# Optimization experiments

Measured on AMD Instinct MI355X. Metric: run time of the kernel, lower is better.

Reference implementation:

```python
import jax, jax.numpy as jnp
from jax import lax
import numpy as np

B, C_IN, C_OUT, H, MODES, L = 16, 128, 128, 8, 256, 16384
HEAD_IN, HEAD_OUT = C_IN // H, C_OUT // H


def setup_inputs() -> dict:
    key = jax.random.key(0)
    ks = jax.random.split(key, 6)
    init_std = (2.0 / (C_IN + C_OUT)) ** 0.5
    return {
        "x": jax.random.normal(ks[0], (B, C_IN, L), dtype=jnp.float32),
        "weight_re": init_std * jax.random.normal(ks[1], (H, HEAD_IN, HEAD_OUT, MODES), dtype=jnp.float32),
        "weight_im": init_std * jax.random.normal(ks[2], (H, HEAD_IN, HEAD_OUT, MODES), dtype=jnp.float32),
        "bias": init_std * jax.random.normal(ks[3], (C_OUT, 1), dtype=jnp.float32),
        "conv_w": (1.0 / np.sqrt(C_IN * 3)) * jax.random.normal(ks[4], (C_OUT, C_IN, 3), dtype=jnp.float32),
        "conv_b": (1.0 / np.sqrt(C_IN * 3)) * jax.random.normal(ks[5], (C_OUT,), dtype=jnp.float32),
        "gate": jnp.array(0.0, dtype=jnp.float32),
    }


def reference(x, weight_re, weight_im, bias, conv_w, conv_b, gate):
    b, _, n = x.shape
    # rfft with norm='forward' (forward transform scaled by 1/n)
    x_freq = jnp.fft.rfft(x, axis=-1, norm="forward")            # (b, C_IN, n//2+1) complex
    x_freq = x_freq.reshape(b, H, HEAD_IN, -1)                    # (b, h, i, f)
    w = weight_re + 1j * weight_im                                # (h, i, o, MODES)
    # truncated low-frequency complex mixing per head
    out_freq = jnp.einsum("bhif,hiof->bhof", x_freq[..., :MODES], w)
    out_freq = out_freq.reshape(b, C_OUT, MODES)
    # irfft zero-pads the truncated spectrum back to n//2+1 modes
    x_out = jnp.fft.irfft(out_freq, n=n, axis=-1, norm="forward")  # (b, C_OUT, n) real
    x_out = x_out + bias                                           # bias: (C_OUT, 1)
    # local conv branch: Conv1d(kernel=3, padding=1) == SAME
    local = lax.conv_general_dilated(
        x, conv_w, window_strides=(1,), padding="SAME",
        dimension_numbers=("NCH", "OIH", "NCH"),
    ) + conv_b[None, :, None]
    g = jax.nn.sigmoid(gate)
    return g * x_out + (1.0 - g) * local
```

## Files before the change

kernel.cpp:

```cpp
#include <hip/hip_runtime.h>


typedef __bf16 bf16x8 __attribute__((ext_vector_type(8)));
typedef __bf16 bf16x4 __attribute__((ext_vector_type(4)));
typedef float f32x4 __attribute__((ext_vector_type(4)));
typedef unsigned short ushort8v __attribute__((ext_vector_type(8)));

#define PI2_OVER_L 3.8349519697141029073e-4f

__global__ void genF_kern(__bf16* __restrict__ Fjt) {
    unsigned idx = blockIdx.x * 256u + threadIdx.x;
    unsigned k = idx >> 14, t = idx & 16383u;
    unsigned m = (k * t) & 16383u;
    float th = (float)m * PI2_OVER_L;
    float s, c;
    __sincosf(th, &s, &c);
    const float inv = 1.0f / 16384.0f;
    Fjt[((size_t)(2u * k) << 14) + t]      = (__bf16)(c * inv);
    Fjt[((size_t)(2u * k + 1u) << 14) + t] = (__bf16)(-s * inv);
}

__global__ void genG_kern(__bf16* __restrict__ Gtj, const float* __restrict__ gate, int fold) {
    unsigned idx = blockIdx.x * 256u + threadIdx.x;
    unsigned t = idx >> 8, k = idx & 255u;
    unsigned m = (k * t) & 16383u;
    float th = (float)m * PI2_OVER_L;
    float s, c;
    __sincosf(th, &s, &c);
    float a = (k == 0u) ? 1.0f : 2.0f;
    if (fold) a *= 1.0f / (1.0f + __expf(-gate[0]));
    size_t base = ((size_t)t << 9) + 2u * k;
    Gtj[base]     = (__bf16)(a * c);
    Gtj[base + 1] = (__bf16)(-a * s);
}

__global__ void wcvt_kern(const float* __restrict__ cw, __bf16* __restrict__ wbf,
                          const float* __restrict__ gate, int fold) {
    int idx = blockIdx.x * 256 + threadIdx.x;
    float sc = 1.0f;
    if (fold) sc = 1.0f - 1.0f / (1.0f + __expf(-gate[0]));
    int co = idx / 384, r = idx - co * 384, ci = r / 3, d = r - ci * 3;
    wbf[d * 16384 + co * 128 + ci] = (__bf16)(cw[idx] * sc);
}

__global__ __launch_bounds__(256) void xpose_kern(const float* __restrict__ x,
        __bf16* __restrict__ xb, __bf16* __restrict__ xTb, int write_xb) {
    __shared__ __bf16 tile[128 * 68];
    int bid = blockIdx.x;
    int b = bid >> 8, tB = bid & 255, t0 = tB << 6;
    int tid = threadIdx.x;
    for (int idx = tid; idx < 2048; idx += 256) {
        int ci = idx >> 4, ch = idx & 15;
        size_t gp = ((size_t)((b << 7) + ci) << 14) + t0 + (ch << 2);
        float4 v = *(const float4*)(x + gp);
        bf16x4 p;
        p[0] = (__bf16)v.x; p[1] = (__bf16)v.y; p[2] = (__bf16)v.z; p[3] = (__bf16)v.w;
        *(bf16x4*)&tile[ci * 68 + (ch << 2)] = p;
        if (write_xb) *(bf16x4*)(xb + gp) = p;
    }
    __syncthreads();
    for (int idx = tid; idx < 1024; idx += 256) {
        int t = idx >> 4, ch = idx & 15;
        bf16x8 v;
#pragma unroll
        for (int j = 0; j < 8; j++) v[j] = tile[(ch * 8 + j) * 68 + t];
        *(bf16x8*)(xTb + (((size_t)(b << 14)) + t0 + t) * 128 + ch * 8) = v;
    }
}

#define SA 72
template<int ABF>
__global__ __launch_bounds__(256) void fwd_kern(const float* __restrict__ xf,
        const __bf16* __restrict__ xbv, const __bf16* __restrict__ Fjt,
        float* __restrict__ Cp, int kchunk) {
    __shared__ __align__(16) __bf16 As[128 * SA];
    __shared__ __align__(16) __bf16 Bs[128 * SA];
    int bid = blockIdx.x;
    int mt = bid & 15, nt = (bid >> 4) & 3, ks = bid >> 6;
    int tid = threadIdx.x, lane = tid & 63, wv = tid >> 6;
    int wm = (wv >> 1) << 6, wn = (wv & 1) << 6;
    f32x4 acc[4][4] = {};
    int arow = tid >> 1, ahalf = (tid & 1) << 5;
    const float*  agf = xf  + ((size_t)(mt * 128 + arow) << 14) + ahalf;
    const __bf16* agb = xbv + ((size_t)(mt * 128 + arow) << 14) + ahalf;
    const __bf16* bg  = Fjt + ((size_t)(nt * 128 + arow) << 14) + ahalf;
    __bf16* ad = &As[arow * SA + ahalf];
    __bf16* bd = &Bs[arow * SA + ahalf];
    int k0 = ks * kchunk;
    for (int kk = 0; kk < kchunk; kk += 64) {
        if (ABF) {
            const ushort8v* ap = (const ushort8v*)(agb + k0 + kk);
#pragma unroll
            for (int q = 0; q < 4; q++) ((ushort8v*)ad)[q] = ap[q];
        } else {
            const float4* ap = (const float4*)(agf + k0 + kk);
#pragma unroll
            for (int q = 0; q < 8; q++) {
                float4 v = ap[q];
                ad[q * 4 + 0] = (__bf16)v.x; ad[q * 4 + 1] = (__bf16)v.y;
                ad[q * 4 + 2] = (__bf16)v.z; ad[q * 4 + 3] = (__bf16)v.w;
            }
        }
        const ushort8v* bp = (const ushort8v*)(bg + k0 + kk);
#pragma unroll
        for (int q = 0; q < 4; q++) ((ushort8v*)bd)[q] = bp[q];
        __syncthreads();
#pragma unroll
        for (int ks2 = 0; ks2 < 64; ks2 += 32) {
            int kf = ks2 + ((lane >> 4) << 3);
            bf16x8 af[4], bfv[4];
#pragma unroll
            for (int i = 0; i < 4; i++)
                af[i] = *(const bf16x8*)&As[(wm + i * 16 + (lane & 15)) * SA + kf];
#pragma unroll
            for (int j = 0; j < 4; j++)
                bfv[j] = *(const bf16x8*)&Bs[(wn + j * 16 + (lane & 15)) * SA + kf];
#pragma unroll
            for (int i = 0; i < 4; i++)
#pragma unroll
                for (int j = 0; j < 4; j++)
                    acc[i][j] = __builtin_amdgcn_mfma_f32_16x16x32_bf16(af[i], bfv[j], acc[i][j], 0, 0, 0);
        }
        __syncthreads();
    }
    float* outp = Cp + (size_t)ks * (2048 * 512);
    int q = lane >> 4, cl = lane & 15;
#pragma unroll
    for (int i = 0; i < 4; i++)
#pragma unroll
        for (int j = 0; j < 4; j++) {
            int col = nt * 128 + wn + j * 16 + cl;
#pragma unroll
            for (int r = 0; r < 4; r++) {
                int row = mt * 128 + wm + i * 16 + q * 4 + r;
                outp[(size_t)row * 512 + col] = acc[i][j][r];
            }
        }
}

__global__ __launch_bounds__(256) void mix_kern(const float* __restrict__ Cp,
        const float* __restrict__ wre, const float* __restrict__ wim,
        __bf16* __restrict__ Ob, int ns) {
    __shared__ float Fs[16 * 256];
    int bid = blockIdx.x, bh = bid >> 1, kh = bid & 1;
    int b = bh >> 3, h = bh & 7;
    int tid = threadIdx.x;
    size_t base = (size_t)(b * 128 + h * 16) * 512 + kh * 256;
    for (int idx = tid; idx < 4096; idx += 256) {
        int i = idx >> 8, jj = idx & 255;
        float v = 0.f;
        for (int s = 0; s < ns; s++) v += Cp[(size_t)s * 1048576 + base + (size_t)i * 512 + jj];
        Fs[i * 256 + jj] = v;
    }
    __syncthreads();
    for (int idx = tid; idx < 2048; idx += 256) {
        int o = idx >> 7, kl = idx & 127;
        int k = kh * 128 + kl;
        float ar = 0.f, ai = 0.f;
        const float* wr0 = wre + ((size_t)(h * 256 + o) << 8) + k;
        const float* wi0 = wim + ((size_t)(h * 256 + o) << 8) + k;
#pragma unroll 4
        for (int i = 0; i < 16; i++) {
            float fr = Fs[i * 256 + 2 * kl], fi = Fs[i * 256 + 2 * kl + 1];
            float wr = wr0[(size_t)i * 4096], wi = wi0[(size_t)i * 4096];
            ar += fr * wr - fi * wi;
            ai += fr * wi + fi * wr;
        }
        size_t ro = (size_t)(b * 128 + h * 16 + o) * 512;
        Ob[ro + 2 * k]     = (__bf16)ar;
        Ob[ro + 2 * k + 1] = (__bf16)ai;
    }
}

#define SC 72
__global__ __launch_bounds__(256) void fused_kern(const __bf16* __restrict__ Ob,
        const __bf16* __restrict__ Gtj, const __bf16* __restrict__ wbf,
        const __bf16* __restrict__ xTb, const float* __restrict__ bias,
        const float* __restrict__ cb, const float* __restrict__ gate,
        float* __restrict__ out) {
    __shared__ __align__(16) char smem[37152];
    int bid = blockIdx.x, b = bid & 15, tt = bid >> 4;
    int t0 = tt << 7;
    int tid = threadIdx.x, lane = tid & 63, wv = tid >> 6;
    int wm = (wv >> 1) << 6, wn = (wv & 1) << 6, lm = lane & 15;
    f32x4 acc[4][4] = {};

    {
        __bf16* As = (__bf16*)smem;
        __bf16* Bs = (__bf16*)(smem + 128 * SA * 2);
        int arow = tid >> 1, ahalf = (tid & 1) << 5;
        const __bf16* ag = Ob  + (size_t)(b * 128 + arow) * 512 + ahalf;
        const __bf16* bg = Gtj + (size_t)(tt * 128 + arow) * 512 + ahalf;
        __bf16* ad = &As[arow * SA + ahalf];
        __bf16* bd = &Bs[arow * SA + ahalf];
        for (int k0 = 0; k0 < 512; k0 += 64) {
#pragma unroll
            for (int q = 0; q < 4; q++) {
                ((ushort8v*)ad)[q] = ((const ushort8v*)(ag + k0))[q];
                ((ushort8v*)bd)[q] = ((const ushort8v*)(bg + k0))[q];
            }
            __syncthreads();
#pragma unroll
            for (int ks2 = 0; ks2 < 64; ks2 += 32) {
                int kf = ks2 + ((lane >> 4) << 3);
                bf16x8 af[4], bfv[4];
#pragma unroll
                for (int i = 0; i < 4; i++)
                    af[i] = *(const bf16x8*)&As[(wm + i * 16 + lm) * SA + kf];
#pragma unroll
                for (int j = 0; j < 4; j++)
                    bfv[j] = *(const bf16x8*)&Bs[(wn + j * 16 + lm) * SA + kf];
#pragma unroll
                for (int i = 0; i < 4; i++)
#pragma unroll
                    for (int j = 0; j < 4; j++)
                        acc[i][j] = __builtin_amdgcn_mfma_f32_16x16x32_bf16(af[i], bfv[j], acc[i][j], 0, 0, 0);
            }
            __syncthreads();
        }
    }

    {
        __bf16* xT = (__bf16*)smem;
        __bf16* Ws = (__bf16*)(smem + 130 * SC * 2);
        for (int c0p = 0; c0p < 2; c0p++) {
            int c0 = c0p << 6;
            if (c0p) __syncthreads();
            for (int idx = tid; idx < 1040; idx += 256) {
                int row = idx >> 3, ch = idx & 7;
                int tg = t0 - 1 + row;
                ushort8v v = {};
                if (tg >= 0 && tg < 16384)
                    v = *(const ushort8v*)(xTb + (((size_t)(b << 14)) + tg) * 128 + c0 + ch * 8);
                *(ushort8v*)&xT[row * SC + ch * 8] = v;
            }
            for (int d = 0; d < 3; d++) {
                if (d) __syncthreads();
                for (int idx = tid; idx < 1024; idx += 256) {
                    int co = idx >> 3, ch = idx & 7;
                    *(ushort8v*)&Ws[co * SC + ch * 8] =
                        *(const ushort8v*)(wbf + d * 16384 + co * 128 + c0 + ch * 8);
                }
                __syncthreads();
#pragma unroll
                for (int ks2 = 0; ks2 < 64; ks2 += 32) {
                    int kf = ks2 + ((lane >> 4) << 3);
                    bf16x8 af[4], bfv[4];
#pragma unroll
                    for (int i = 0; i < 4; i++)
                        af[i] = *(const bf16x8*)&Ws[(wm + i * 16 + lm) * SC + kf];
#pragma unroll
                    for (int j = 0; j < 4; j++)
                        bfv[j] = *(const bf16x8*)&xT[(wn + j * 16 + lm + d) * SC + kf];
#pragma unroll
                    for (int i = 0; i < 4; i++)
#pragma unroll
                        for (int j = 0; j < 4; j++)
                            acc[i][j] = __builtin_amdgcn_mfma_f32_16x16x32_bf16(af[i], bfv[j], acc[i][j], 0, 0, 0);
                }
            }
        }
    }

    float g = 1.0f / (1.0f + __expf(-gate[0]));
    int q = lane >> 4, cl = lane & 15;
#pragma unroll
    for (int i = 0; i < 4; i++)
#pragma unroll
        for (int j = 0; j < 4; j++) {
            int t = t0 + wn + j * 16 + cl;
#pragma unroll
            for (int r = 0; r < 4; r++) {
                int co = wm + i * 16 + q * 4 + r;
                float gb = g * bias[co] + (1.0f - g) * cb[co];
                out[((size_t)(b * 128 + co) << 14) + t] = acc[i][j][r] + gb;
            }
        }
}

#define SXC 40
__global__ __launch_bounds__(256) void conv_kern(const float* __restrict__ x,
        const __bf16* __restrict__ wbf, const float* __restrict__ cb,
        float* __restrict__ out) {
    __shared__ __align__(16) __bf16 xT[130 * SXC];
    __shared__ __align__(16) __bf16 wS[3 * 128 * SXC];
    int bid = blockIdx.x, b = bid >> 7, t0 = (bid & 127) << 7;
    int tid = threadIdx.x, lane = tid & 63, wv = tid >> 6;
    int wm = (wv >> 1) << 6, wn = (wv & 1) << 6;
    f32x4 acc[4][4] = {};
    for (int c0 = 0; c0 < 128; c0 += 32) {
        for (int idx = tid; idx < 1536; idx += 256) {
            int d = idx / 512, rem = idx - d * 512, co = rem >> 2, g = rem & 3;
            ushort8v v = *(const ushort8v*)(wbf + d * 16384 + co * 128 + c0 + g * 8);
            *(ushort8v*)&wS[d * (128 * SXC) + co * SXC + g * 8] = v;
        }
        for (int idx = tid; idx < 4160; idx += 256) {
            int cc = idx / 130, tl = idx - cc * 130;
            int tg = t0 + tl - 1;
            float v = 0.f;
            if (tg >= 0 && tg < 16384)
                v = x[((size_t)(b * 128 + c0 + cc) << 14) + tg];
            xT[tl * SXC + cc] = (__bf16)v;
        }
        __syncthreads();
        int kf = (lane >> 4) << 3;
#pragma unroll
        for (int d = 0; d < 3; d++) {
            bf16x8 af[4], bfv[4];
#pragma unroll
            for (int i = 0; i < 4; i++)
                af[i] = *(const bf16x8*)&wS[d * (128 * SXC) + (wm + i * 16 + (lane & 15)) * SXC + kf];
#pragma unroll
            for (int j = 0; j < 4; j++)
                bfv[j] = *(const bf16x8*)&xT[(wn + j * 16 + (lane & 15) + d) * SXC + kf];
#pragma unroll
            for (int i = 0; i < 4; i++)
#pragma unroll
                for (int j = 0; j < 4; j++)
                    acc[i][j] = __builtin_amdgcn_mfma_f32_16x16x32_bf16(af[i], bfv[j], acc[i][j], 0, 0, 0);
        }
        __syncthreads();
    }
    int q = lane >> 4, cl = lane & 15;
#pragma unroll
    for (int i = 0; i < 4; i++)
#pragma unroll
        for (int j = 0; j < 4; j++) {
            int t = t0 + wn + j * 16 + cl;
#pragma unroll
            for (int r = 0; r < 4; r++) {
                int co = wm + i * 16 + q * 4 + r;
                out[((size_t)(b * 128 + co) << 14) + t] = acc[i][j][r] + cb[co];
            }
        }
}

__global__ __launch_bounds__(256) void inv_kern(const __bf16* __restrict__ Ob,
        const __bf16* __restrict__ Gtj, const float* __restrict__ bias,
        const float* __restrict__ gate, float* __restrict__ out) {
    __shared__ __align__(16) __bf16 As[128 * SA];
    __shared__ __align__(16) __bf16 Bs[128 * SA];
    int bid = blockIdx.x, mt = bid & 15, tt = bid >> 4;
    int tid = threadIdx.x, lane = tid & 63, wv = tid >> 6;
    int wm = (wv >> 1) << 6, wn = (wv & 1) << 6;
    f32x4 acc[4][4] = {};
    int arow = tid >> 1, ahalf = (tid & 1) << 5;
    const __bf16* ag = Ob  + (size_t)(mt * 128 + arow) * 512 + ahalf;
    const __bf16* bg = Gtj + (size_t)(tt * 128 + arow) * 512 + ahalf;
    __bf16* ad = &As[arow * SA + ahalf];
    __bf16* bd = &Bs[arow * SA + ahalf];
    for (int k0 = 0; k0 < 512; k0 += 64) {
#pragma unroll
        for (int q = 0; q < 4; q++) {
            ((ushort8v*)ad)[q] = ((const ushort8v*)(ag + k0))[q];
            ((ushort8v*)bd)[q] = ((const ushort8v*)(bg + k0))[q];
        }
        __syncthreads();
#pragma unroll
        for (int ks2 = 0; ks2 < 64; ks2 += 32) {
            int kf = ks2 + ((lane >> 4) << 3);
            bf16x8 af[4], bfv[4];
#pragma unroll
            for (int i = 0; i < 4; i++)
                af[i] = *(const bf16x8*)&As[(wm + i * 16 + (lane & 15)) * SA + kf];
#pragma unroll
            for (int j = 0; j < 4; j++)
                bfv[j] = *(const bf16x8*)&Bs[(wn + j * 16 + (lane & 15)) * SA + kf];
#pragma unroll
            for (int i = 0; i < 4; i++)
#pragma unroll
                for (int j = 0; j < 4; j++)
                    acc[i][j] = __builtin_amdgcn_mfma_f32_16x16x32_bf16(af[i], bfv[j], acc[i][j], 0, 0, 0);
        }
        __syncthreads();
    }
    float g = 1.0f / (1.0f + __expf(-gate[0]));
    float gi = 1.0f - g;
    int q = lane >> 4, cl = lane & 15;
#pragma unroll
    for (int i = 0; i < 4; i++)
#pragma unroll
        for (int j = 0; j < 4; j++) {
            int col = (tt << 7) + wn + j * 16 + cl;
#pragma unroll
            for (int r = 0; r < 4; r++) {
                int row = mt * 128 + wm + i * 16 + q * 4 + r;
                size_t oi = ((size_t)row << 14) + col;
                out[oi] = g * (acc[i][j][r] + bias[row & 127]) + gi * out[oi];
            }
        }
}

extern "C" void kernel_launch(void* const* d_in, const int* in_sizes, int n_in,
                              void* d_out, int out_size, void* d_ws, size_t ws_size,
                              hipStream_t stream) {
    const float* x    = (const float*)d_in[0];
    const float* wre  = (const float*)d_in[1];
    const float* wim  = (const float*)d_in[2];
    const float* bias = (const float*)d_in[3];
    const float* cw   = (const float*)d_in[4];
    const float* cb   = (const float*)d_in[5];
    const float* gate = (const float*)d_in[6];
    float* out = (float*)d_out;
    char* ws = (char*)d_ws;

    const size_t SZ_F = 16777216, SZ_G = 16777216, SZ_W = 98304;
    const size_t SZ_X = 67108864, SZ_CP8 = 33554432, SZ_CP4 = 16777216, SZ_OB = 2097152;
    size_t oG = SZ_F, oW = oG + SZ_G, oEnd = oW + SZ_W;

    size_t needT3 = oEnd + 2 * SZ_X + SZ_CP8 + SZ_OB;
    size_t needT2 = oEnd + SZ_X + SZ_CP8 + SZ_OB;
    size_t needT1 = oEnd + SZ_X + SZ_CP4 + SZ_OB;

    __bf16* Fjt = (__bf16*)(ws);
    __bf16* Gtj = (__bf16*)(ws + oG);
    __bf16* wbf = (__bf16*)(ws + oW);

    if (ws_size >= needT1) {
        int use_xb = (ws_size >= needT3);
        int ns = (ws_size >= needT2) ? 8 : 4;
        __bf16* xb  = use_xb ? (__bf16*)(ws + oEnd) : nullptr;
        __bf16* xTb = (__bf16*)(ws + oEnd + (use_xb ? SZ_X : 0));
        float*  Cp  = (float*)((char*)xTb + SZ_X);
        __bf16* Ob  = (__bf16*)((char*)Cp + (size_t)ns * 4194304);
        int kchunk = 16384 / ns;

        genF_kern<<<16384, 256, 0, stream>>>(Fjt);
        genG_kern<<<16384, 256, 0, stream>>>(Gtj, gate, 1);
        wcvt_kern<<<192, 256, 0, stream>>>(cw, wbf, gate, 1);
        xpose_kern<<<4096, 256, 0, stream>>>(x, xb, xTb, use_xb);
        if (use_xb)
            fwd_kern<1><<<64 * ns, 256, 0, stream>>>(x, xb, Fjt, Cp, kchunk);
        else
            fwd_kern<0><<<64 * ns, 256, 0, stream>>>(x, nullptr, Fjt, Cp, kchunk);
        mix_kern<<<256, 256, 0, stream>>>(Cp, wre, wim, Ob, ns);
        fused_kern<<<2048, 256, 0, stream>>>(Ob, Gtj, wbf, xTb, bias, cb, gate, out);
    } else {
        float*  Cp  = (float*)(ws + oEnd);
        size_t need8 = oEnd + 8ull * 4194304ull + SZ_OB;
        int ns = (ws_size >= need8) ? 8 : 4;
        __bf16* Ob  = (__bf16*)(ws + oEnd + (size_t)ns * 4194304);
        int kchunk = 16384 / ns;

        genF_kern<<<16384, 256, 0, stream>>>(Fjt);
        genG_kern<<<16384, 256, 0, stream>>>(Gtj, gate, 0);
        wcvt_kern<<<192, 256, 0, stream>>>(cw, wbf, gate, 0);
        fwd_kern<0><<<64 * ns, 256, 0, stream>>>(x, nullptr, Fjt, Cp, kchunk);
        mix_kern<<<256, 256, 0, stream>>>(Cp, wre, wim, Ob, ns);
        conv_kern<<<2048, 256, 0, stream>>>(x, wbf, cb, out);
        inv_kern<<<2048, 256, 0, stream>>>(Ob, Gtj, bias, gate, out);
    }
}
```

Baseline: 520.9 us.

## Use direct global-to-LDS loads with XOR-swizzled tiles and merge generator kernels

Merges the three twiddle and weight generation kernels into a single launch. The GEMM stages (forward DFT and the fused inverse-plus-conv kernel) now stage operand tiles with global_load_lds 16-byte loads into unpadded, XOR-swizzled LDS, replacing register round-trips and padded layouts. The transpose tile is swizzled the same way, and the mix reduction uses vectorized float4 loads. The aim is lower launch overhead, fewer VGPR staging copies and fewer bank conflicts. The price is more complex addressing and reliance on the LDS-DMA builtin's lane-to-address mapping being correct.

```diff
diff --git a/kernel.cpp b/kernel.cpp
--- a/kernel.cpp
+++ b/kernel.cpp
@@ -8,44 +8,49 @@
 
 #define PI2_OVER_L 3.8349519697141029073e-4f
 
-__global__ void genF_kern(__bf16* __restrict__ Fjt) {
-    unsigned idx = blockIdx.x * 256u + threadIdx.x;
-    unsigned k = idx >> 14, t = idx & 16383u;
-    unsigned m = (k * t) & 16383u;
-    float th = (float)m * PI2_OVER_L;
-    float s, c;
-    __sincosf(th, &s, &c);
-    const float inv = 1.0f / 16384.0f;
-    Fjt[((size_t)(2u * k) << 14) + t]      = (__bf16)(c * inv);
-    Fjt[((size_t)(2u * k + 1u) << 14) + t] = (__bf16)(-s * inv);
-}
-
-__global__ void genG_kern(__bf16* __restrict__ Gtj, const float* __restrict__ gate, int fold) {
-    unsigned idx = blockIdx.x * 256u + threadIdx.x;
-    unsigned t = idx >> 8, k = idx & 255u;
-    unsigned m = (k * t) & 16383u;
-    float th = (float)m * PI2_OVER_L;
-    float s, c;
-    __sincosf(th, &s, &c);
-    float a = (k == 0u) ? 1.0f : 2.0f;
-    if (fold) a *= 1.0f / (1.0f + __expf(-gate[0]));
-    size_t base = ((size_t)t << 9) + 2u * k;
-    Gtj[base]     = (__bf16)(a * c);
-    Gtj[base + 1] = (__bf16)(-a * s);
-}
-
-__global__ void wcvt_kern(const float* __restrict__ cw, __bf16* __restrict__ wbf,
-                          const float* __restrict__ gate, int fold) {
-    int idx = blockIdx.x * 256 + threadIdx.x;
-    float sc = 1.0f;
-    if (fold) sc = 1.0f - 1.0f / (1.0f + __expf(-gate[0]));
-    int co = idx / 384, r = idx - co * 384, ci = r / 3, d = r - ci * 3;
-    wbf[d * 16384 + co * 128 + ci] = (__bf16)(cw[idx] * sc);
+#define GLD16(gp, lp) __builtin_amdgcn_global_load_lds( \
+    (const __attribute__((address_space(1))) void*)(gp), \
+    (__attribute__((address_space(3))) void*)(lp), 16, 0, 0)
+
+
+__global__ void gen_kern(__bf16* __restrict__ Fjt, __bf16* __restrict__ Gtj,
+                         const float* __restrict__ cw, __bf16* __restrict__ wbf,
+                         const float* __restrict__ gate, int fold) {
+    unsigned bid = blockIdx.x;
+    if (bid < 16384u) {
+        unsigned idx = bid * 256u + threadIdx.x;
+        unsigned k = idx >> 14, t = idx & 16383u;
+        unsigned m = (k * t) & 16383u;
+        float th = (float)m * PI2_OVER_L;
+        float s, c;
+        __sincosf(th, &s, &c);
+        const float inv = 1.0f / 16384.0f;
+        Fjt[((size_t)(2u * k) << 14) + t]      = (__bf16)(c * inv);
+        Fjt[((size_t)(2u * k + 1u) << 14) + t] = (__bf16)(-s * inv);
+    } else if (bid < 32768u) {
+        unsigned idx = (bid - 16384u) * 256u + threadIdx.x;
+        unsigned t = idx >> 8, k = idx & 255u;
+        unsigned m = (k * t) & 16383u;
+        float th = (float)m * PI2_OVER_L;
+        float s, c;
+        __sincosf(th, &s, &c);
+        float a = (k == 0u) ? 1.0f : 2.0f;
+        if (fold) a *= 1.0f / (1.0f + __expf(-gate[0]));
+        size_t base = ((size_t)t << 9) + 2u * k;
+        Gtj[base]     = (__bf16)(a * c);
+        Gtj[base + 1] = (__bf16)(-a * s);
+    } else {
+        int idx = (int)(bid - 32768u) * 256 + threadIdx.x;
+        float sc = 1.0f;
+        if (fold) sc = 1.0f - 1.0f / (1.0f + __expf(-gate[0]));
+        int co = idx / 384, r = idx - co * 384, ci = r / 3, d = r - ci * 3;
+        wbf[d * 16384 + co * 128 + ci] = (__bf16)(cw[idx] * sc);
+    }
 }
 
 __global__ __launch_bounds__(256) void xpose_kern(const float* __restrict__ x,
         __bf16* __restrict__ xb, __bf16* __restrict__ xTb, int write_xb) {
-    __shared__ __bf16 tile[128 * 68];
+    __shared__ __align__(16) __bf16 tile[128 * 64];
     int bid = blockIdx.x;
     int b = bid >> 8, tB = bid & 255, t0 = tB << 6;
     int tid = threadIdx.x;
@@ -55,7 +60,7 @@
         float4 v = *(const float4*)(x + gp);
         bf16x4 p;
         p[0] = (__bf16)v.x; p[1] = (__bf16)v.y; p[2] = (__bf16)v.z; p[3] = (__bf16)v.w;
-        *(bf16x4*)&tile[ci * 68 + (ch << 2)] = p;
+        *(bf16x4*)((char*)tile + (ci << 7) + (((ch >> 1) ^ ((ci >> 3) & 7)) << 4) + ((ch & 1) << 3)) = p;
         if (write_xb) *(bf16x4*)(xb + gp) = p;
     }
     __syncthreads();
@@ -63,58 +68,67 @@
         int t = idx >> 4, ch = idx & 15;
         bf16x8 v;
 #pragma unroll
-        for (int j = 0; j < 8; j++) v[j] = tile[(ch * 8 + j) * 68 + t];
+        for (int j = 0; j < 8; j++) {
+            int ci = (ch << 3) + j;
+            v[j] = *(const __bf16*)((char*)tile + (ci << 7) +
+                     ((((t >> 3) ^ ((ci >> 3) & 7))) << 4) + ((t & 7) << 1));
+        }
         *(bf16x8*)(xTb + (((size_t)(b << 14)) + t0 + t) * 128 + ch * 8) = v;
     }
 }
 
-#define SA 72
 template<int ABF>
 __global__ __launch_bounds__(256) void fwd_kern(const float* __restrict__ xf,
         const __bf16* __restrict__ xbv, const __bf16* __restrict__ Fjt,
         float* __restrict__ Cp, int kchunk) {
-    __shared__ __align__(16) __bf16 As[128 * SA];
-    __shared__ __align__(16) __bf16 Bs[128 * SA];
+    __shared__ __align__(16) char smem[32768];
     int bid = blockIdx.x;
     int mt = bid & 15, nt = (bid >> 4) & 3, ks = bid >> 6;
     int tid = threadIdx.x, lane = tid & 63, wv = tid >> 6;
-    int wm = (wv >> 1) << 6, wn = (wv & 1) << 6;
+    int wm = (wv >> 1) << 6, wn = (wv & 1) << 6, lm = lane & 15;
+    int rx = lm & 7;
+    int r8 = lane >> 3, c8 = lane & 7;
+    int srcoff = (c8 ^ r8) << 3;
+    int ldrow = (wv << 5) + r8;
+    char* ldst = smem + (wv << 12);
     f32x4 acc[4][4] = {};
-    int arow = tid >> 1, ahalf = (tid & 1) << 5;
-    const float*  agf = xf  + ((size_t)(mt * 128 + arow) << 14) + ahalf;
-    const __bf16* agb = xbv + ((size_t)(mt * 128 + arow) << 14) + ahalf;
-    const __bf16* bg  = Fjt + ((size_t)(nt * 128 + arow) << 14) + ahalf;
-    __bf16* ad = &As[arow * SA + ahalf];
-    __bf16* bd = &Bs[arow * SA + ahalf];
     int k0 = ks * kchunk;
+    const __bf16* ag = xbv + (((size_t)(mt * 128 + ldrow)) << 14) + k0 + srcoff;
+    const __bf16* bg = Fjt + (((size_t)(nt * 128 + ldrow)) << 14) + k0 + srcoff;
+    int frow = tid >> 1;
+    const float* agf = xf + (((size_t)(mt * 128 + frow)) << 14) + k0;
     for (int kk = 0; kk < kchunk; kk += 64) {
         if (ABF) {
-            const ushort8v* ap = (const ushort8v*)(agb + k0 + kk);
-#pragma unroll
-            for (int q = 0; q < 4; q++) ((ushort8v*)ad)[q] = ap[q];
+#pragma unroll
+            for (int q = 0; q < 4; q++)
+                GLD16(ag + (((size_t)q) << 17) + kk, ldst + (q << 10));
         } else {
-            const float4* ap = (const float4*)(agf + k0 + kk);
-#pragma unroll
-            for (int q = 0; q < 8; q++) {
-                float4 v = ap[q];
-                ad[q * 4 + 0] = (__bf16)v.x; ad[q * 4 + 1] = (__bf16)v.y;
-                ad[q * 4 + 2] = (__bf16)v.z; ad[q * 4 + 3] = (__bf16)v.w;
-            }
-        }
-        const ushort8v* bp = (const ushort8v*)(bg + k0 + kk);
-#pragma unroll
-        for (int q = 0; q < 4; q++) ((ushort8v*)bd)[q] = bp[q];
+#pragma unroll
+            for (int q = 0; q < 4; q++) {
+                int sl = ((tid & 1) << 2) + q;
+                const float4* p = (const float4*)(agf + kk + (sl << 3));
+                float4 v0 = p[0], v1 = p[1];
+                bf16x8 t;
+                t[0] = (__bf16)v0.x; t[1] = (__bf16)v0.y; t[2] = (__bf16)v0.z; t[3] = (__bf16)v0.w;
+                t[4] = (__bf16)v1.x; t[5] = (__bf16)v1.y; t[6] = (__bf16)v1.z; t[7] = (__bf16)v1.w;
+                *(bf16x8*)(smem + (frow << 7) + ((sl ^ (frow & 7)) << 4)) = t;
+            }
+        }
+#pragma unroll
+        for (int q = 0; q < 4; q++)
+            GLD16(bg + (((size_t)q) << 17) + kk, ldst + 16384 + (q << 10));
         __syncthreads();
 #pragma unroll
         for (int ks2 = 0; ks2 < 64; ks2 += 32) {
-            int kf = ks2 + ((lane >> 4) << 3);
+            int wb = (ks2 >> 3) + (lane >> 4);
+            int wa = (wb ^ rx) << 4;
             bf16x8 af[4], bfv[4];
 #pragma unroll
             for (int i = 0; i < 4; i++)
-                af[i] = *(const bf16x8*)&As[(wm + i * 16 + (lane & 15)) * SA + kf];
+                af[i] = *(const bf16x8*)(smem + ((wm + i * 16 + lm) << 7) + wa);
 #pragma unroll
             for (int j = 0; j < 4; j++)
-                bfv[j] = *(const bf16x8*)&Bs[(wn + j * 16 + (lane & 15)) * SA + kf];
+                bfv[j] = *(const bf16x8*)(smem + 16384 + ((wn + j * 16 + lm) << 7) + wa);
 #pragma unroll
             for (int i = 0; i < 4; i++)
 #pragma unroll
@@ -141,16 +155,18 @@
 __global__ __launch_bounds__(256) void mix_kern(const float* __restrict__ Cp,
         const float* __restrict__ wre, const float* __restrict__ wim,
         __bf16* __restrict__ Ob, int ns) {
-    __shared__ float Fs[16 * 256];
+    __shared__ __align__(16) float Fs[16 * 256];
     int bid = blockIdx.x, bh = bid >> 1, kh = bid & 1;
     int b = bh >> 3, h = bh & 7;
     int tid = threadIdx.x;
     size_t base = (size_t)(b * 128 + h * 16) * 512 + kh * 256;
-    for (int idx = tid; idx < 4096; idx += 256) {
-        int i = idx >> 8, jj = idx & 255;
-        float v = 0.f;
-        for (int s = 0; s < ns; s++) v += Cp[(size_t)s * 1048576 + base + (size_t)i * 512 + jj];
-        Fs[i * 256 + jj] = v;
+    for (int idx = tid; idx < 1024; idx += 256) {
+        int i = idx >> 6, jj = (idx & 63) << 2;
+        const float* p = Cp + base + (size_t)i * 512 + jj;
+        f32x4 v = {};
+#pragma unroll 4
+        for (int s = 0; s < ns; s++) v += *(const f32x4*)(p + (size_t)s * 1048576);
+        *(f32x4*)&Fs[i * 256 + jj] = v;
     }
     __syncthreads();
     for (int idx = tid; idx < 2048; idx += 256) {
@@ -172,44 +188,44 @@
     }
 }
 
-#define SC 72
 __global__ __launch_bounds__(256) void fused_kern(const __bf16* __restrict__ Ob,
         const __bf16* __restrict__ Gtj, const __bf16* __restrict__ wbf,
         const __bf16* __restrict__ xTb, const float* __restrict__ bias,
         const float* __restrict__ cb, const float* __restrict__ gate,
         float* __restrict__ out) {
-    __shared__ __align__(16) char smem[37152];
+    __shared__ __align__(16) char smem[33024];
     int bid = blockIdx.x, b = bid & 15, tt = bid >> 4;
     int t0 = tt << 7;
     int tid = threadIdx.x, lane = tid & 63, wv = tid >> 6;
     int wm = (wv >> 1) << 6, wn = (wv & 1) << 6, lm = lane & 15;
+    int rx = lm & 7;
+    int r8 = lane >> 3, c8 = lane & 7;
+    int srcoff = (c8 ^ r8) << 3;
+    int ldrow = (wv << 5) + r8;
+    char* ldst = smem + (wv << 12);
     f32x4 acc[4][4] = {};
 
     {
-        __bf16* As = (__bf16*)smem;
-        __bf16* Bs = (__bf16*)(smem + 128 * SA * 2);
-        int arow = tid >> 1, ahalf = (tid & 1) << 5;
-        const __bf16* ag = Ob  + (size_t)(b * 128 + arow) * 512 + ahalf;
-        const __bf16* bg = Gtj + (size_t)(tt * 128 + arow) * 512 + ahalf;
-        __bf16* ad = &As[arow * SA + ahalf];
-        __bf16* bd = &Bs[arow * SA + ahalf];
+        const __bf16* ag = Ob  + ((size_t)(b  * 128 + ldrow) << 9) + srcoff;
+        const __bf16* bg = Gtj + ((size_t)(tt * 128 + ldrow) << 9) + srcoff;
         for (int k0 = 0; k0 < 512; k0 += 64) {
 #pragma unroll
             for (int q = 0; q < 4; q++) {
-                ((ushort8v*)ad)[q] = ((const ushort8v*)(ag + k0))[q];
-                ((ushort8v*)bd)[q] = ((const ushort8v*)(bg + k0))[q];
+                GLD16(ag + ((size_t)q << 12) + k0, ldst + (q << 10));
+                GLD16(bg + ((size_t)q << 12) + k0, ldst + 16384 + (q << 10));
             }
             __syncthreads();
 #pragma unroll
             for (int ks2 = 0; ks2 < 64; ks2 += 32) {
-                int kf = ks2 + ((lane >> 4) << 3);
+                int wb = (ks2 >> 3) + (lane >> 4);
+                int wa = (wb ^ rx) << 4;
                 bf16x8 af[4], bfv[4];
 #pragma unroll
                 for (int i = 0; i < 4; i++)
-                    af[i] = *(const bf16x8*)&As[(wm + i * 16 + lm) * SA + kf];
+                    af[i] = *(const bf16x8*)(smem + ((wm + i * 16 + lm) << 7) + wa);
 #pragma unroll
                 for (int j = 0; j < 4; j++)
-                    bfv[j] = *(const bf16x8*)&Bs[(wn + j * 16 + lm) * SA + kf];
+                    bfv[j] = *(const bf16x8*)(smem + 16384 + ((wn + j * 16 + lm) << 7) + wa);
 #pragma unroll
                 for (int i = 0; i < 4; i++)
 #pragma unroll
@@ -221,8 +237,7 @@
     }
 
     {
-        __bf16* xT = (__bf16*)smem;
-        __bf16* Ws = (__bf16*)(smem + 130 * SC * 2);
+        char* xT = smem + 16384;
         for (int c0p = 0; c0p < 2; c0p++) {
             int c0 = c0p << 6;
             if (c0p) __syncthreads();
@@ -231,27 +246,29 @@
                 int tg = t0 - 1 + row;
                 ushort8v v = {};
                 if (tg >= 0 && tg < 16384)
-                    v = *(const ushort8v*)(xTb + (((size_t)(b << 14)) + tg) * 128 + c0 + ch * 8);
-                *(ushort8v*)&xT[row * SC + ch * 8] = v;
-            }
+                    v = *(const ushort8v*)(xTb + ((((size_t)(b << 14)) + tg) << 7) + c0 + (ch << 3));
+                *(ushort8v*)(xT + (row << 7) + ((ch ^ (row & 7)) << 4)) = v;
+            }
+            const __bf16* wg = wbf + (ldrow << 7) + c0 + srcoff;
             for (int d = 0; d < 3; d++) {
                 if (d) __syncthreads();
-                for (int idx = tid; idx < 1024; idx += 256) {
-                    int co = idx >> 3, ch = idx & 7;
-                    *(ushort8v*)&Ws[co * SC + ch * 8] =
-                        *(const ushort8v*)(wbf + d * 16384 + co * 128 + c0 + ch * 8);
-                }
+#pragma unroll
+                for (int q = 0; q < 4; q++)
+                    GLD16(wg + d * 16384 + (q << 10), ldst + (q << 10));
                 __syncthreads();
 #pragma unroll
                 for (int ks2 = 0; ks2 < 64; ks2 += 32) {
-                    int kf = ks2 + ((lane >> 4) << 3);
+                    int wb = (ks2 >> 3) + (lane >> 4);
+                    int wa = (wb ^ rx) << 4;
                     bf16x8 af[4], bfv[4];
 #pragma unroll
                     for (int i = 0; i < 4; i++)
-                        af[i] = *(const bf16x8*)&Ws[(wm + i * 16 + lm) * SC + kf];
-#pragma unroll
-                    for (int j = 0; j < 4; j++)
-                        bfv[j] = *(const bf16x8*)&xT[(wn + j * 16 + lm + d) * SC + kf];
+                        af[i] = *(const bf16x8*)(smem + ((wm + i * 16 + lm) << 7) + wa);
+#pragma unroll
+                    for (int j = 0; j < 4; j++) {
+                        int r2 = wn + j * 16 + lm + d;
+                        bfv[j] = *(const bf16x8*)(xT + (r2 << 7) + ((wb ^ (r2 & 7)) << 4));
+                    }
 #pragma unroll
                     for (int i = 0; i < 4; i++)
 #pragma unroll
@@ -278,6 +295,7 @@
         }
 }
 
+#define SA 72
 #define SXC 40
 __global__ __launch_bounds__(256) void conv_kern(const float* __restrict__ x,
         const __bf16* __restrict__ wbf, const float* __restrict__ cb,
@@ -425,9 +443,7 @@
         __bf16* Ob  = (__bf16*)((char*)Cp + (size_t)ns * 4194304);
         int kchunk = 16384 / ns;
 
-        genF_kern<<<16384, 256, 0, stream>>>(Fjt);
-        genG_kern<<<16384, 256, 0, stream>>>(Gtj, gate, 1);
-        wcvt_kern<<<192, 256, 0, stream>>>(cw, wbf, gate, 1);
+        gen_kern<<<32960, 256, 0, stream>>>(Fjt, Gtj, cw, wbf, gate, 1);
         xpose_kern<<<4096, 256, 0, stream>>>(x, xb, xTb, use_xb);
         if (use_xb)
             fwd_kern<1><<<64 * ns, 256, 0, stream>>>(x, xb, Fjt, Cp, kchunk);
@@ -442,9 +458,7 @@
         __bf16* Ob  = (__bf16*)(ws + oEnd + (size_t)ns * 4194304);
         int kchunk = 16384 / ns;
 
-        genF_kern<<<16384, 256, 0, stream>>>(Fjt);
-        genG_kern<<<16384, 256, 0, stream>>>(Gtj, gate, 0);
-        wcvt_kern<<<192, 256, 0, stream>>>(cw, wbf, gate, 0);
+        gen_kern<<<32960, 256, 0, stream>>>(Fjt, Gtj, cw, wbf, gate, 0);
         fwd_kern<0><<<64 * ns, 256, 0, stream>>>(x, nullptr, Fjt, Cp, kchunk);
         mix_kern<<<256, 256, 0, stream>>>(Cp, wre, wim, Ob, ns);
         conv_kern<<<2048, 256, 0, stream>>>(x, wbf, cb, out);
```

Result: faster. 458.5 us (-12.0%).
